# Optimization experiments

Measured on AMD Instinct MI355X. Metric: run time of the kernel, lower is better.

## Reference

```python
import jax, jax.numpy as jnp
import numpy as np

NUM_EMBEDDINGS = 512
EMBEDDING_DIM = 256
COMMITMENT_COST = 0.5
DECAY = 0.99
EPSILON = 1e-05


def setup_inputs() -> dict:
    key = jax.random.key(0)
    k1, k2, k3 = jax.random.split(key, 3)
    z_e = jax.random.normal(k1, (16, 256, 16, 16, 16), dtype=jnp.float32)
    codebook = jax.random.normal(k2, (NUM_EMBEDDINGS, EMBEDDING_DIM), dtype=jnp.float32)
    ema_cluster_size = jnp.ones((NUM_EMBEDDINGS,), dtype=jnp.float32)
    ema_embed_sum = jax.random.normal(k3, (NUM_EMBEDDINGS, EMBEDDING_DIM), dtype=jnp.float32)
    return {"z_e": z_e, "codebook": codebook,
            "ema_cluster_size": ema_cluster_size, "ema_embed_sum": ema_embed_sum}


def reference(z_e, codebook, ema_cluster_size, ema_embed_sum):
    B, C, D, H, W = z_e.shape
    K = codebook.shape[0]
    # [B, D, H, W, C] -> [N, C]
    z_perm = jnp.transpose(z_e, (0, 2, 3, 4, 1))
    flat = z_perm.reshape(-1, C)

    # squared-distance argmin: ||z||^2 + ||e||^2 - 2 z.e  (N x K)
    z_sq = jnp.sum(flat * flat, axis=1, keepdims=True)          # [N, 1]
    e_sq = jnp.sum(codebook * codebook, axis=1)[None, :]        # [1, K]
    dot = flat @ codebook.T                                      # [N, K]
    distances = z_sq + e_sq - 2.0 * dot
    encoding_indices = jnp.argmin(distances, axis=1)             # [N]

    z_q_flat = codebook[encoding_indices]                        # gather lookup

    # EMA statistics (training-mode buffer updates; dead-code reset omitted
    # since it is driven by a host-side randperm).
    batch_cluster_size = jax.ops.segment_sum(
        jnp.ones_like(encoding_indices, dtype=flat.dtype), encoding_indices,
        num_segments=K)
    batch_embed_sum = jax.ops.segment_sum(flat, encoding_indices, num_segments=K)
    new_cluster_size = DECAY * ema_cluster_size + (1.0 - DECAY) * batch_cluster_size
    new_embed_sum = DECAY * ema_embed_sum + (1.0 - DECAY) * batch_embed_sum
    n = jnp.sum(new_cluster_size)
    smoothed = (new_cluster_size + EPSILON) / (n + K * EPSILON) * n
    new_codebook = new_embed_sum / smoothed[:, None]

    z_q_perm = z_q_flat.reshape(z_perm.shape)
    commitment_loss = jnp.mean((z_perm - jax.lax.stop_gradient(z_q_perm)) ** 2)
    vq_loss = COMMITMENT_COST * commitment_loss

    # straight-through estimator
    z_q_st = z_perm + jax.lax.stop_gradient(z_q_perm - z_perm)
    z_q = jnp.transpose(z_q_st, (0, 4, 1, 2, 3))
    indices_out = encoding_indices.reshape(B, D, H, W)
    return (z_q, vq_loss, indices_out, new_codebook, new_cluster_size, new_embed_sum)
```

## Files before the change

### kernel.cpp

```cpp
#include <hip/hip_runtime.h>
#include <cfloat>

#define K_NUM 512
#define C_DIM 256

#define WS_CNT    0
#define WS_ESQ    512
#define WS_SMOOTH 1024
#define WS_LOSS   1536
#define WS_CBT    2048
#define WS_ACC    133120

#define OFF_LOSS 16777216
#define OFF_IDX  16777217
#define OFF_CB   16842753
#define OFF_CS   16973825
#define OFF_ES   16974337

__global__ __launch_bounds__(256) void k0a_prep(const float* __restrict__ cb,
                                                float* __restrict__ ws) {
  int k = blockIdx.x, c = threadIdx.x;
  float v = cb[k * C_DIM + c];
  float s = v * v;
  #pragma unroll
  for (int o = 32; o > 0; o >>= 1) s += __shfl_down(s, o, 64);
  __shared__ float ls[4];
  if ((c & 63) == 0) ls[c >> 6] = s;
  __syncthreads();
  if (c == 0) {
    ws[WS_ESQ + k] = ls[0] + ls[1] + ls[2] + ls[3];
    ws[WS_CNT + k] = 0.f;
    if (k == 0) ws[WS_LOSS] = 0.f;
  }
}

__global__ __launch_bounds__(256) void k0b_transpose(const float* __restrict__ cb,
                                                     float* __restrict__ cbT) {
  __shared__ float t[64 * 69];
  int tid = threadIdx.x;
  int k0 = (blockIdx.x >> 2) * 64;
  int c0 = (blockIdx.x & 3) * 64;
  {
    int kk = tid >> 4, cq = tid & 15;
    #pragma unroll
    for (int r = 0; r < 4; ++r) {
      int row = kk + 16 * r;
      float4 v = *(const float4*)&cb[(size_t)(k0 + row) * C_DIM + c0 + 4 * cq];
      float* p = &t[row * 69 + 4 * cq];
      p[0] = v.x; p[1] = v.y; p[2] = v.z; p[3] = v.w;
    }
  }
  __syncthreads();
  {
    int kq = tid & 15, cc = tid >> 4;
    #pragma unroll
    for (int r = 0; r < 4; ++r) {
      int c = cc + 16 * r;
      float4 v;
      v.x = t[(4 * kq + 0) * 69 + c];
      v.y = t[(4 * kq + 1) * 69 + c];
      v.z = t[(4 * kq + 2) * 69 + c];
      v.w = t[(4 * kq + 3) * 69 + c];
      *(float4*)&cbT[(size_t)(c0 + c) * K_NUM + k0 + 4 * kq] = v;
    }
  }
}

__global__ __launch_bounds__(256)
__attribute__((amdgpu_waves_per_eu(2, 4)))
void k1_gemm(const float* __restrict__ z,
             const float* __restrict__ cb,
             float* __restrict__ out,
             float* __restrict__ ws) {
  __shared__ __align__(16) float zt[32 * 132];
  __shared__ __align__(16) float ct[32 * 128];
  __shared__ __align__(16) int   s_fidx[128];
  __shared__ float s_fmv[128];
  __shared__ float s_ls[4];

  const float* cbT = ws + WS_CBT;
  const float* esq = ws + WS_ESQ;

  int tid = threadIdx.x;
  int nb = blockIdx.x << 7;
  int b = nb >> 12;
  int d = (nb >> 8) & 15;
  int off = nb & 255;
  size_t base = (size_t)b * 1048576 + (size_t)d * 256 + off;
  const float* zbase = z + base;

  int wn = tid >> 4;
  int wk = tid & 15;

  float minv[8]; int mini[8];
  #pragma unroll
  for (int i = 0; i < 8; ++i) { minv[i] = FLT_MAX; mini[i] = 0; }

  for (int kc = 0; kc < 4; ++kc) {
    float acc[8][8];
    #pragma unroll
    for (int i = 0; i < 8; ++i)
      #pragma unroll
      for (int j = 0; j < 8; ++j) acc[i][j] = 0.f;

    for (int c4 = 0; c4 < 8; ++c4) {
      int c0 = c4 * 32;
      __syncthreads();
      #pragma unroll
      for (int r = 0; r < 4; ++r) {
        int idx4 = tid + 256 * r;
        int cc = idx4 >> 5, j4 = idx4 & 31;
        float4 v = *(const float4*)(zbase + (size_t)(c0 + cc) * 4096 + 4 * j4);
        *(float4*)&zt[cc * 132 + 4 * j4] = v;
      }
      #pragma unroll
      for (int r = 0; r < 4; ++r) {
        int idx4 = tid + 256 * r;
        int cc = idx4 >> 5, k4 = idx4 & 31;
        float4 v = *(const float4*)(cbT + (size_t)(c0 + cc) * K_NUM + kc * 128 + 4 * k4);
        *(float4*)&ct[cc * 128 + 4 * k4] = v;
      }
      __syncthreads();
      #pragma unroll 4
      for (int cc = 0; cc < 32; ++cc) {
        float4 za = *(const float4*)&zt[cc * 132 + 4 * wn];
        float4 zb = *(const float4*)&zt[cc * 132 + 64 + 4 * wn];
        float4 ca = *(const float4*)&ct[cc * 128 + 4 * wk];
        float4 cb4 = *(const float4*)&ct[cc * 128 + 64 + 4 * wk];
        float zr[8] = {za.x, za.y, za.z, za.w, zb.x, zb.y, zb.z, zb.w};
        float cr[8] = {ca.x, ca.y, ca.z, ca.w, cb4.x, cb4.y, cb4.z, cb4.w};
        #pragma unroll
        for (int i = 0; i < 8; ++i)
          #pragma unroll
          for (int j = 0; j < 8; ++j) acc[i][j] += zr[i] * cr[j];
      }
    }
    #pragma unroll
    for (int j = 0; j < 8; ++j) {
      int kg = kc * 128 + (j >> 2) * 64 + 4 * wk + (j & 3);
      float er = esq[kg];
      #pragma unroll
      for (int i = 0; i < 8; ++i) {
        float val = er - 2.f * acc[i][j];
        if (val < minv[i] || (val == minv[i] && kg < mini[i])) { minv[i] = val; mini[i] = kg; }
      }
    }
  }
  #pragma unroll
  for (int i = 0; i < 8; ++i) {
    float v = minv[i]; int ii = mini[i];
    #pragma unroll
    for (int o = 8; o > 0; o >>= 1) {
      float ov = __shfl_xor(v, o, 16);
      int   oi = __shfl_xor(ii, o, 16);
      if (ov < v || (ov == v && oi < ii)) { v = ov; ii = oi; }
    }
    if (wk == i) {
      int n = (i >> 2) * 64 + 4 * wn + (i & 3);
      s_fidx[n] = ii; s_fmv[n] = v;
      out[OFF_IDX + nb + n] = (float)ii;
    }
  }
  __syncthreads();
  int j4 = (tid & 31) * 4;
  int ch = tid >> 5;
  int4 idxs = *(const int4*)&s_fidx[j4];
  const float* r0 = cb + (size_t)idxs.x * C_DIM;
  const float* r1 = cb + (size_t)idxs.y * C_DIM;
  const float* r2 = cb + (size_t)idxs.z * C_DIM;
  const float* r3 = cb + (size_t)idxs.w * C_DIM;
  float zsq = 0.f;
  #pragma unroll 4
  for (int i = 0; i < 32; ++i) {
    int c = ch + 8 * i;
    float4 zv = *(const float4*)(zbase + (size_t)c * 4096 + j4);
    float4 q = make_float4(r0[c], r1[c], r2[c], r3[c]);
    *(float4*)(out + base + (size_t)c * 4096 + j4) = q;
    zsq += zv.x * zv.x + zv.y * zv.y + zv.z * zv.z + zv.w * zv.w;
  }
  if (tid < 128) zsq += s_fmv[tid];
  #pragma unroll
  for (int o = 32; o > 0; o >>= 1) zsq += __shfl_down(zsq, o, 64);
  if ((tid & 63) == 0) s_ls[tid >> 6] = zsq;
  __syncthreads();
  if (tid == 0) unsafeAtomicAdd(&ws[WS_LOSS], s_ls[0] + s_ls[1] + s_ls[2] + s_ls[3]);
}

__global__ __launch_bounds__(256) void k1b_scatter(const float* __restrict__ z,
                                                   const float* __restrict__ out,
                                                   float* __restrict__ ws, int n_per) {
  __shared__ float tab[K_NUM * 65];
  float* counts = ws + WS_CNT;
  float* myTab = ws + WS_ACC + (size_t)blockIdx.x * (K_NUM * C_DIM);

  int tid = threadIdx.x;
  int nb = blockIdx.x * n_per;

  for (int pass = 0; pass < 4; ++pass) {
    int cq = pass * 64;
    for (int i = tid; i < K_NUM * 65; i += 256) tab[i] = 0.f;
    __syncthreads();

    for (int nn = tid * 4; nn < n_per; nn += 1024) {
      int n0 = nb + nn;
      int i0 = (int)out[OFF_IDX + n0 + 0];
      int i1 = (int)out[OFF_IDX + n0 + 1];
      int i2 = (int)out[OFF_IDX + n0 + 2];
      int i3 = (int)out[OFF_IDX + n0 + 3];
      if (pass == 0) {
        unsafeAtomicAdd(&counts[i0], 1.f);
        unsafeAtomicAdd(&counts[i1], 1.f);
        unsafeAtomicAdd(&counts[i2], 1.f);
        unsafeAtomicAdd(&counts[i3], 1.f);
      }
      int a0 = i0 * 65, a1 = i1 * 65, a2 = i2 * 65, a3 = i3 * 65;
      size_t basez = (size_t)(n0 >> 12) * 1048576 + (size_t)(n0 & 4095);
      const float* zp = z + basez + (size_t)cq * 4096;
      #pragma unroll 8
      for (int cl = 0; cl < 64; ++cl) {
        float4 zv = *(const float4*)(zp + (size_t)cl * 4096);
        atomicAdd(&tab[a0 + cl], zv.x);
        atomicAdd(&tab[a1 + cl], zv.y);
        atomicAdd(&tab[a2 + cl], zv.z);
        atomicAdd(&tab[a3 + cl], zv.w);
      }
    }
    __syncthreads();
    int cl = tid & 63, kr = tid >> 6;
    for (int k0 = 0; k0 < K_NUM; k0 += 4) {
      int k = k0 + kr;
      myTab[k * C_DIM + cq + cl] = tab[k * 65 + cl];
    }
    __syncthreads();
  }
}

__global__ __launch_bounds__(512) void k2_cluster(const float* __restrict__ ema_cs,
                                                  float* __restrict__ out,
                                                  float* __restrict__ ws) {
  int k = threadIdx.x;
  float ncs = 0.99f * ema_cs[k] + 0.01f * ws[WS_CNT + k];
  out[OFF_CS + k] = ncs;
  float s = ncs;
  #pragma unroll
  for (int o = 32; o > 0; o >>= 1) s += __shfl_down(s, o, 64);
  __shared__ float ls[8];
  __shared__ float ntot;
  if ((k & 63) == 0) ls[k >> 6] = s;
  __syncthreads();
  if (k == 0) {
    float n = 0.f;
    #pragma unroll
    for (int i = 0; i < 8; ++i) n += ls[i];
    ntot = n;
    out[OFF_LOSS] = 0.5f * ws[WS_LOSS] / 16777216.f;
  }
  __syncthreads();
  float n = ntot;
  ws[WS_SMOOTH + k] = (ncs + 1e-5f) / (n + 0.00512f) * n;
}

__global__ __launch_bounds__(256) void k3_embed(const float* __restrict__ ema_es,
                                                float* __restrict__ out,
                                                const float* __restrict__ ws, int nblk) {
  int k = blockIdx.x, c = threadIdx.x;
  int i = k * C_DIM + c;
  float bs = 0.f;
  for (int t = 0; t < nblk; ++t) bs += ws[WS_ACC + (size_t)t * (K_NUM * C_DIM) + i];
  float es = 0.99f * ema_es[i] + 0.01f * bs;
  out[OFF_ES + i] = es;
  out[OFF_CB + i] = es / ws[WS_SMOOTH + k];
}

extern "C" void kernel_launch(void* const* d_in, const int* in_sizes, int n_in,
                              void* d_out, int out_size, void* d_ws, size_t ws_size,
                              hipStream_t stream) {
  const float* z      = (const float*)d_in[0];
  const float* cb     = (const float*)d_in[1];
  const float* ema_cs = (const float*)d_in[2];
  const float* ema_es = (const float*)d_in[3];
  float* out = (float*)d_out;
  float* ws  = (float*)d_ws;

  size_t avail = ws_size / 4;
  int nblk = 128;
  while (nblk > 8 && (size_t)WS_ACC + (size_t)nblk * (K_NUM * C_DIM) > avail) nblk >>= 1;
  int n_per = 65536 / nblk;

  k0a_prep<<<512, 256, 0, stream>>>(cb, ws);
  k0b_transpose<<<32, 256, 0, stream>>>(cb, ws + WS_CBT);
  k1_gemm<<<512, 256, 0, stream>>>(z, cb, out, ws);
  k1b_scatter<<<nblk, 256, 0, stream>>>(z, out, ws, n_per);
  k2_cluster<<<1, 512, 0, stream>>>(ema_cs, out, ws);
  k3_embed<<<512, 256, 0, stream>>>(ema_es, out, ws, nblk);
}
```

Before: 663.0 us.

## Stage full z tile in LDS via async loads and double-buffer codebook tiles

The GEMM kernel now loads the whole 256x128 z tile into LDS once with global_load_lds, and double-buffers 16-row codebook tiles so the next tile is fetched while the current one is computed. The epilogue reads z from LDS instead of re-reading global memory. The scatter kernel switches to float2 loads with workgroup-scoped relaxed LDS atomics. The trade-off is far more LDS per block (about 144 KB), which lowers occupancy, and the waves_per_eu hint is dropped.

```diff
diff --git a/kernel.cpp b/kernel.cpp
--- a/kernel.cpp
+++ b/kernel.cpp
@@ -16,6 +16,12 @@
 #define OFF_CB   16842753
 #define OFF_CS   16973825
 #define OFF_ES   16974337
+
+__device__ __forceinline__ void gl_lds16(const float* g, float* l) {
+  __builtin_amdgcn_global_load_lds(
+      (const __attribute__((address_space(1))) unsigned int*)g,
+      (__attribute__((address_space(3))) unsigned int*)l, 16, 0, 0);
+}
 
 __global__ __launch_bounds__(256) void k0a_prep(const float* __restrict__ cb,
                                                 float* __restrict__ ws) {
@@ -66,14 +72,23 @@
   }
 }
 
-__global__ __launch_bounds__(256)
-__attribute__((amdgpu_waves_per_eu(2, 4)))
-void k1_gemm(const float* __restrict__ z,
-             const float* __restrict__ cb,
-             float* __restrict__ out,
-             float* __restrict__ ws) {
-  __shared__ __align__(16) float zt[32 * 132];
-  __shared__ __align__(16) float ct[32 * 128];
+#define STAGE_CT(buf, skc, sc8) do {                                          \
+    int c0_ = (sc8) << 4;                                                     \
+    _Pragma("unroll")                                                         \
+    for (int r_ = 0; r_ < 2; ++r_) {                                          \
+      int i4_ = tid + (r_ << 8);                                              \
+      gl_lds16(cbT + ((size_t)(c0_ + (i4_ >> 5)) << 9) + ((skc) << 7)         \
+                   + ((i4_ & 31) << 2),                                       \
+               &ct[((buf) << 11) + (i4_ << 2)]);                              \
+    }                                                                         \
+  } while (0)
+
+__global__ __launch_bounds__(256) void k1_gemm(const float* __restrict__ z,
+                                               const float* __restrict__ cb,
+                                               float* __restrict__ out,
+                                               float* __restrict__ ws) {
+  __shared__ __align__(16) float zt[256 * 128];
+  __shared__ __align__(16) float ct[2 * 16 * 128];
   __shared__ __align__(16) int   s_fidx[128];
   __shared__ float s_fmv[128];
   __shared__ float s_ls[4];
@@ -92,10 +107,20 @@
   int wn = tid >> 4;
   int wk = tid & 15;
 
+  #pragma unroll 8
+  for (int r = 0; r < 32; ++r) {
+    int idx4 = tid + (r << 8);
+    gl_lds16(zbase + ((size_t)(idx4 >> 5) << 12) + ((idx4 & 31) << 2),
+             &zt[idx4 << 2]);
+  }
+  STAGE_CT(0, 0, 0);
+  __syncthreads();
+
   float minv[8]; int mini[8];
   #pragma unroll
   for (int i = 0; i < 8; ++i) { minv[i] = FLT_MAX; mini[i] = 0; }
 
+  int cur = 0;
   for (int kc = 0; kc < 4; ++kc) {
     float acc[8][8];
     #pragma unroll
@@ -103,30 +128,17 @@
       #pragma unroll
       for (int j = 0; j < 8; ++j) acc[i][j] = 0.f;
 
-    for (int c4 = 0; c4 < 8; ++c4) {
-      int c0 = c4 * 32;
-      __syncthreads();
-      #pragma unroll
-      for (int r = 0; r < 4; ++r) {
-        int idx4 = tid + 256 * r;
-        int cc = idx4 >> 5, j4 = idx4 & 31;
-        float4 v = *(const float4*)(zbase + (size_t)(c0 + cc) * 4096 + 4 * j4);
-        *(float4*)&zt[cc * 132 + 4 * j4] = v;
-      }
-      #pragma unroll
-      for (int r = 0; r < 4; ++r) {
-        int idx4 = tid + 256 * r;
-        int cc = idx4 >> 5, k4 = idx4 & 31;
-        float4 v = *(const float4*)(cbT + (size_t)(c0 + cc) * K_NUM + kc * 128 + 4 * k4);
-        *(float4*)&ct[cc * 128 + 4 * k4] = v;
-      }
-      __syncthreads();
+    for (int c8 = 0; c8 < 16; ++c8) {
+      int nc8 = c8 + 1, nkc = kc + (nc8 >> 4); nc8 &= 15;
+      if (nkc < 4) STAGE_CT(cur ^ 1, nkc, nc8);
+      const float* ctb = &ct[cur << 11];
       #pragma unroll 4
-      for (int cc = 0; cc < 32; ++cc) {
-        float4 za = *(const float4*)&zt[cc * 132 + 4 * wn];
-        float4 zb = *(const float4*)&zt[cc * 132 + 64 + 4 * wn];
-        float4 ca = *(const float4*)&ct[cc * 128 + 4 * wk];
-        float4 cb4 = *(const float4*)&ct[cc * 128 + 64 + 4 * wk];
+      for (int cc = 0; cc < 16; ++cc) {
+        int c = (c8 << 4) + cc;
+        float4 za = *(const float4*)&zt[c * 128 + 4 * wn];
+        float4 zb = *(const float4*)&zt[c * 128 + 64 + 4 * wn];
+        float4 ca = *(const float4*)&ctb[cc * 128 + 4 * wk];
+        float4 cb4 = *(const float4*)&ctb[cc * 128 + 64 + 4 * wk];
         float zr[8] = {za.x, za.y, za.z, za.w, zb.x, zb.y, zb.z, zb.w};
         float cr[8] = {ca.x, ca.y, ca.z, ca.w, cb4.x, cb4.y, cb4.z, cb4.w};
         #pragma unroll
@@ -134,6 +146,8 @@
           #pragma unroll
           for (int j = 0; j < 8; ++j) acc[i][j] += zr[i] * cr[j];
       }
+      __syncthreads();
+      cur ^= 1;
     }
     #pragma unroll
     for (int j = 0; j < 8; ++j) {
@@ -173,7 +187,7 @@
   #pragma unroll 4
   for (int i = 0; i < 32; ++i) {
     int c = ch + 8 * i;
-    float4 zv = *(const float4*)(zbase + (size_t)c * 4096 + j4);
+    float4 zv = *(const float4*)&zt[c * 128 + j4];
     float4 q = make_float4(r0[c], r1[c], r2[c], r3[c]);
     *(float4*)(out + base + (size_t)c * 4096 + j4) = q;
     zsq += zv.x * zv.x + zv.y * zv.y + zv.z * zv.z + zv.w * zv.w;
@@ -201,28 +215,24 @@
     for (int i = tid; i < K_NUM * 65; i += 256) tab[i] = 0.f;
     __syncthreads();
 
-    for (int nn = tid * 4; nn < n_per; nn += 1024) {
+    for (int nn = tid * 2; nn < n_per; nn += 512) {
       int n0 = nb + nn;
-      int i0 = (int)out[OFF_IDX + n0 + 0];
+      int i0 = (int)out[OFF_IDX + n0];
       int i1 = (int)out[OFF_IDX + n0 + 1];
-      int i2 = (int)out[OFF_IDX + n0 + 2];
-      int i3 = (int)out[OFF_IDX + n0 + 3];
       if (pass == 0) {
         unsafeAtomicAdd(&counts[i0], 1.f);
         unsafeAtomicAdd(&counts[i1], 1.f);
-        unsafeAtomicAdd(&counts[i2], 1.f);
-        unsafeAtomicAdd(&counts[i3], 1.f);
       }
-      int a0 = i0 * 65, a1 = i1 * 65, a2 = i2 * 65, a3 = i3 * 65;
+      int a0 = i0 * 65, a1 = i1 * 65;
       size_t basez = (size_t)(n0 >> 12) * 1048576 + (size_t)(n0 & 4095);
       const float* zp = z + basez + (size_t)cq * 4096;
       #pragma unroll 8
       for (int cl = 0; cl < 64; ++cl) {
-        float4 zv = *(const float4*)(zp + (size_t)cl * 4096);
-        atomicAdd(&tab[a0 + cl], zv.x);
-        atomicAdd(&tab[a1 + cl], zv.y);
-        atomicAdd(&tab[a2 + cl], zv.z);
-        atomicAdd(&tab[a3 + cl], zv.w);
+        float2 zv = *(const float2*)(zp + (size_t)cl * 4096);
+        __hip_atomic_fetch_add(&tab[a0 + cl], zv.x, __ATOMIC_RELAXED,
+                               __HIP_MEMORY_SCOPE_WORKGROUP);
+        __hip_atomic_fetch_add(&tab[a1 + cl], zv.y, __ATOMIC_RELAXED,
+                               __HIP_MEMORY_SCOPE_WORKGROUP);
       }
     }
     __syncthreads();
```

Result: slower. 699.0 us (+5.4%).
